# Kernel optimization log

Measured on AMD Instinct MI355X. Metric: run time of the kernel, lower is better.

The kernel has to match this reference:

```python
import jax, jax.numpy as jnp
import numpy as np

THETA_ALPHA = 160.0  # spatial bandwidth of bilateral kernel
THETA_BETA = 3.0     # color bandwidth of bilateral kernel
THETA_GAMMA = 3.0    # spatial bandwidth of spatial kernel
NUM_ITERS = 5        # mean-field iterations


def setup_inputs() -> dict:
    key = jax.random.key(0)
    ks = jax.random.split(key, 5)
    B, H, W, C = 1, 80, 80, 21
    unaries = jax.random.normal(ks[0], (B, H, W, C), dtype=jnp.float32)
    image = jax.random.uniform(ks[1], (B, H, W, 3), dtype=jnp.float32) * 255.0
    spatial_w = jax.random.normal(ks[2], (C, C), dtype=jnp.float32) * 0.1 + jnp.eye(C)
    bilateral_w = jax.random.normal(ks[3], (C, C), dtype=jnp.float32) * 0.1 + jnp.eye(C)
    compat = jax.random.normal(ks[4], (C, C), dtype=jnp.float32) * 0.1 - jnp.eye(C)
    return {"unaries": unaries, "image": image, "spatial_w": spatial_w,
            "bilateral_w": bilateral_w, "compat": compat}


def _gauss_kernel(feat):
    # feat: [N, F] -> dense Gaussian affinity exp(-0.5*||f_i - f_j||^2), [N, N]
    sq = jnp.sum(feat * feat, axis=-1)
    d2 = sq[:, None] + sq[None, :] - 2.0 * (feat @ feat.T)
    return jnp.exp(-0.5 * jnp.maximum(d2, 0.0))


def reference(unaries, image, spatial_w, bilateral_w, compat):
    B, H, W, C = unaries.shape
    N = H * W
    yy, xx = jnp.meshgrid(jnp.arange(H, dtype=jnp.float32),
                          jnp.arange(W, dtype=jnp.float32), indexing="ij")
    pos = jnp.stack([yy, xx], axis=-1).reshape(N, 2)          # [N, 2]
    rgb = image.reshape(N, 3)
    feat_s = pos / THETA_GAMMA                                 # spatial kernel features
    feat_b = jnp.concatenate([pos / THETA_ALPHA, rgb / THETA_BETA], axis=-1)
    Ks = _gauss_kernel(feat_s)                                 # [N, N]
    Kb = _gauss_kernel(feat_b)                                 # [N, N]
    norm_s = jnp.sum(Ks, axis=-1, keepdims=True)               # splat-of-ones normalization
    norm_b = jnp.sum(Kb, axis=-1, keepdims=True)
    u = unaries.reshape(N, C)
    q = u
    for _ in range(NUM_ITERS):
        p = jax.nn.softmax(q, axis=-1)                         # [N, C]
        msg = (Ks @ p) / norm_s @ spatial_w.T + (Kb @ p) / norm_b @ bilateral_w.T
        q = u - msg @ compat.T                                 # compatibility transform
    return q.reshape(B, H, W, C)
```

## Files before the change

kernel.cpp:

```cpp
#include <hip/hip_runtime.h>


#define HH 80
#define WW 80
#define NPIX 6400
#define CC 21
#define PP 24
#define NITER 5
#define NCAP 64
#define SCAP 48
#define SADGATE 23u
#define RAD 14

typedef short short8 __attribute__((ext_vector_type(8)));
union H8 { short8 v; unsigned short u[8]; };

__device__ __forceinline__ float bf2f(unsigned short h) {
    return __uint_as_float(((unsigned)h) << 16);
}
__device__ __forceinline__ unsigned short f2bf(float f) {
    unsigned u = __float_as_uint(f);
    return (unsigned short)((u + 0x7fffu + ((u >> 16) & 1u)) >> 16);
}

__global__ void __launch_bounds__(1024) nbr_kernel(const float* __restrict__ image,
        const float* __restrict__ unaries,
        const float* __restrict__ sw, const float* __restrict__ bw,
        const float* __restrict__ ct,
        int* __restrict__ nbr_j, float* __restrict__ nbr_k, int* __restrict__ nbr_cnt,
        float* __restrict__ norm_b, float* __restrict__ Stab,
        float* __restrict__ csw_g, float* __restrict__ cbw_g,
        unsigned short* __restrict__ p0) {
    __shared__ unsigned int cimg[NPIX];
    int tid = threadIdx.x;
    int bid = blockIdx.x;
    for (int px = tid; px < NPIX; px += 1024) {
        float r = image[px * 3 + 0], g = image[px * 3 + 1], b = image[px * 3 + 2];
        unsigned ur = (unsigned)(r + 0.5f), ug = (unsigned)(g + 0.5f), ub = (unsigned)(b + 0.5f);
        cimg[px] = ur | (ug << 8) | (ub << 16);
    }
    if (bid == 0) {
        if (tid < HH) {
            float s = 0.f;
            float t = (float)tid;
            for (int tp = 0; tp < HH; ++tp) {
                float d = t - (float)tp;
                s += __expf(-d * d * (1.0f / 18.0f));
            }
            Stab[tid] = s;
        }
        for (int idx = tid; idx < 2 * CC * CC; idx += 1024) {
            int m = idx % (CC * CC);
            int c = m / CC, k = m % CC;
            const float* wmat = (idx < CC * CC) ? sw : bw;
            float s = 0.f;
            for (int mm = 0; mm < CC; ++mm) s += ct[c * CC + mm] * wmat[mm * CC + k];
            if (idx < CC * CC) csw_g[m] = s; else cbw_g[m] = s;
        }
    }
    __syncthreads();
    int lane = tid & 63;
    int i = bid * 16 + (tid >> 6);
    unsigned ci = cimg[i];
    float eir = image[i * 3 + 0], eig = image[i * 3 + 1], eib = image[i * 3 + 2];
    float yi = (float)(i / WW), xi = (float)(i % WW);
    int base = 0;
    float ksum = 0.f;
    for (int j0 = 0; j0 < NPIX; j0 += 64) {
        int j = j0 + lane;
        unsigned cj = cimg[j];
#if __has_builtin(__builtin_amdgcn_sad_u8)
        unsigned sad = __builtin_amdgcn_sad_u8(ci, cj, 0u);
#else
        int dr = (int)(ci & 255u) - (int)(cj & 255u);
        int dg = (int)((ci >> 8) & 255u) - (int)((cj >> 8) & 255u);
        int db = (int)((ci >> 16) & 255u) - (int)((cj >> 16) & 255u);
        unsigned sad = (unsigned)(abs(dr) + abs(dg) + abs(db));
#endif
        bool pass = (sad <= SADGATE);
        unsigned long long mask = __ballot(pass);
        if (pass) {
            int slot = base + __popcll(mask & ((1ull << lane) - 1ull));
            if (slot < NCAP) {
                float er = eir - image[j * 3 + 0];
                float eg = eig - image[j * 3 + 1];
                float eb = eib - image[j * 3 + 2];
                float dy = (yi - (float)(j / WW)) * (1.0f / 160.0f);
                float dx = (xi - (float)(j % WW)) * (1.0f / 160.0f);
                float d2 = (er * er + eg * eg + eb * eb) * (1.0f / 9.0f) + dy * dy + dx * dx;
                float kk = __expf(-0.5f * d2);
                nbr_j[i * NCAP + slot] = j;
                nbr_k[i * NCAP + slot] = kk;
                ksum += kk;
            }
        }
        base += (int)__popcll(mask);
    }
    for (int off = 32; off > 0; off >>= 1) ksum += __shfl_down(ksum, off, 64);
    if (lane == 0) {
        nbr_cnt[i] = (base < NCAP) ? base : NCAP;
        norm_b[i] = ksum;
    }
    float v = (lane < CC) ? unaries[i * CC + lane] : -1e30f;
    float m = v;
    for (int off = 16; off > 0; off >>= 1) m = fmaxf(m, __shfl_down(m, off, 32));
    m = __shfl(m, 0, 32);
    float e = (lane < CC) ? __expf(v - m) : 0.f;
    float s = e;
    for (int off = 16; off > 0; off >>= 1) s += __shfl_down(s, off, 32);
    s = __shfl(s, 0, 32);
    if (lane < PP) p0[i * PP + lane] = (lane < CC) ? f2bf(e / s) : (unsigned short)0;
}

__global__ void __launch_bounds__(320) iter_kernel(const float* __restrict__ unaries,
        const unsigned short* __restrict__ pc,
        const int* __restrict__ nbr_j, const float* __restrict__ nbr_k,
        const int* __restrict__ nbr_cnt, const float* __restrict__ norm_b,
        const float* __restrict__ Stab,
        const float* __restrict__ csw_g, const float* __restrict__ cbw_g,
        unsigned short* __restrict__ pn, float* __restrict__ out, int last) {
    __shared__ float lcsw[CC * CC], lcbw[CC * CC];
    __shared__ float gl[16];
    __shared__ float cy[38 * PP];
    __shared__ float asb[10 * 25], abb[10 * 25];
    __shared__ int   njl[10][SCAP];
    __shared__ float nkl[10][SCAP];
    __shared__ int   cnt_l[10];
    __shared__ float inv_ns[10];

    int tid = threadIdx.x;
    int y = blockIdx.x >> 3;
    int x0 = (blockIdx.x & 7) * 10;
    int xs = (x0 - RAD > 0) ? x0 - RAD : 0;
    int xe = (x0 + 10 + RAD < WW) ? x0 + 10 + RAD : WW;
    int extw = xe - xs;
    const short8* pc8 = (const short8*)pc;

    for (int idx = tid; idx < 2 * CC * CC; idx += 320) {
        if (idx < CC * CC) lcsw[idx] = csw_g[idx];
        else lcbw[idx - CC * CC] = cbw_g[idx - CC * CC];
    }
    if (tid < 16) { float d = (float)tid; gl[tid] = __expf(-d * d * (1.0f / 18.0f)); }
    if (tid >= 32 && tid < 42) {
        int px = tid - 32;
        int i = y * WW + x0 + px;
        int cnt = nbr_cnt[i]; if (cnt > SCAP) cnt = SCAP;
        cnt_l[px] = cnt;
        inv_ns[px] = 1.0f / (Stab[y] * Stab[x0 + px]);
    }
    for (int idx = tid; idx < 10 * SCAP; idx += 320) {
        int px = idx / SCAP, sl = idx % SCAP;
        int i = y * WW + x0 + px;
        int cnt = nbr_cnt[i]; if (cnt > SCAP) cnt = SCAP;
        if (sl < cnt) {
            njl[px][sl] = nbr_j[i * NCAP + sl];
            nkl[px][sl] = nbr_k[i * NCAP + sl] / norm_b[i];
        }
    }
    __syncthreads();

    if (tid < extw * 3) {
        int col = tid / 3, grp = tid % 3;
        int x = xs + col;
        int ys_ = (y - RAD > 0) ? y - RAD : 0;
        int ye_ = (y + RAD < HH - 1) ? y + RAD : HH - 1;
        float a[8] = {0, 0, 0, 0, 0, 0, 0, 0};
        for (int yp = ys_; yp <= ye_; ++yp) {
            int d = y - yp; if (d < 0) d = -d;
            float g = gl[d];
            H8 h; h.v = pc8[(yp * WW + x) * 3 + grp];
            #pragma unroll
            for (int e = 0; e < 8; ++e) a[e] += g * bf2f(h.u[e]);
        }
        #pragma unroll
        for (int e = 0; e < 8; ++e) cy[col * PP + grp * 8 + e] = a[e];
    }
    __syncthreads();

    int px = tid >> 5, c = tid & 31;
    int x = x0 + px;
    int i = y * WW + x;
    if (c < CC) {
        int q0 = (x - RAD > 0) ? x - RAD : 0;
        int q1 = (x + RAD < WW - 1) ? x + RAD : WW - 1;
        float s = 0.f;
        for (int xp = q0; xp <= q1; ++xp) {
            int d = x - xp; if (d < 0) d = -d;
            s += gl[d] * cy[(xp - xs) * PP + c];
        }
        asb[px * 25 + c] = s * inv_ns[px];
        int cnt = cnt_l[px];
        float ab = 0.f;
        for (int n = 0; n < cnt; ++n)
            ab += nkl[px][n] * bf2f(pc[njl[px][n] * PP + c]);
        abb[px * 25 + c] = ab;
    }
    __syncthreads();

    if (last) {
        if (c < CC) {
            float m = 0.f;
            #pragma unroll
            for (int k = 0; k < CC; ++k)
                m += lcsw[c * CC + k] * asb[px * 25 + k] + lcbw[c * CC + k] * abb[px * 25 + k];
            out[i * CC + c] = unaries[i * CC + c] - m;
        }
    } else {
        float ev = 0.f;
        if (c < CC) {
            float m = 0.f;
            #pragma unroll
            for (int k = 0; k < CC; ++k)
                m += lcsw[c * CC + k] * asb[px * 25 + k] + lcbw[c * CC + k] * abb[px * 25 + k];
            ev = __expf(unaries[i * CC + c] - m);
        }
        float s = ev;
        #pragma unroll
        for (int off = 16; off > 0; off >>= 1) s += __shfl_xor(s, off, 32);
        if (c < CC) pn[i * PP + c] = f2bf(ev / s);
    }
}

extern "C" void kernel_launch(void* const* d_in, const int* in_sizes, int n_in,
                              void* d_out, int out_size, void* d_ws, size_t ws_size,
                              hipStream_t stream) {
    const float* unaries = (const float*)d_in[0];
    const float* image   = (const float*)d_in[1];
    const float* sw      = (const float*)d_in[2];
    const float* bw      = (const float*)d_in[3];
    const float* ct      = (const float*)d_in[4];
    float* out = (float*)d_out;

    char* ws = (char*)d_ws;
    size_t off = 0;
    auto alloc = [&](size_t bytes) -> char* {
        char* p = ws + off;
        off += (bytes + 255) & ~(size_t)255;
        return p;
    };
    int*   nbr_j   = (int*)alloc((size_t)NPIX * NCAP * 4);
    float* nbr_k   = (float*)alloc((size_t)NPIX * NCAP * 4);
    int*   nbr_cnt = (int*)alloc((size_t)NPIX * 4);
    float* norm_b  = (float*)alloc((size_t)NPIX * 4);
    unsigned short* pA = (unsigned short*)alloc((size_t)NPIX * PP * 2);
    unsigned short* pB = (unsigned short*)alloc((size_t)NPIX * PP * 2);
    float* Stab    = (float*)alloc(HH * 4);
    float* csw_g   = (float*)alloc(CC * CC * 4);
    float* cbw_g   = (float*)alloc(CC * CC * 4);
    (void)ws_size;

    nbr_kernel<<<400, 1024, 0, stream>>>(image, unaries, sw, bw, ct,
                                         nbr_j, nbr_k, nbr_cnt, norm_b, Stab,
                                         csw_g, cbw_g, pA);
    unsigned short* pc = pA;
    unsigned short* pn = pB;
    for (int t = 0; t < NITER; ++t) {
        iter_kernel<<<640, 320, 0, stream>>>(unaries, pc, nbr_j, nbr_k, nbr_cnt,
                                             norm_b, Stab, csw_g, cbw_g, pn, out,
                                             (t == NITER - 1) ? 1 : 0);
        unsigned short* tsw = pc; pc = pn; pn = tsw;
    }
}
```

Baseline: 145.7 us.

## Fuse first mean-field iteration into neighbor kernel and shrink neighbor cap

The neighbor-search kernel now also performs the first mean-field iteration. It computes softmax of the unaries on the fly and writes the second-iteration probabilities, so one iteration launch is dropped. The neighbor cap drops from 64 to 32, and normalization is folded into the stored bilateral weights, which removes the norm_b buffer. The iteration kernel now uses 8-pixel tiles with 256 threads, loads neighbor lists into registers and broadcasts them by shuffle, and computes the Gaussian weights with exp instead of a table. The smaller cap may change accuracy for pixels with many neighbors, and the fused first iteration recomputes softmax per neighbor.

```diff
diff --git a/kernel.cpp b/kernel.cpp
--- a/kernel.cpp
+++ b/kernel.cpp
@@ -7,8 +7,7 @@
 #define CC 21
 #define PP 24
 #define NITER 5
-#define NCAP 64
-#define SCAP 48
+#define NCAP 32
 #define SADGATE 23u
 #define RAD 14
 
@@ -23,152 +22,241 @@
     return (unsigned short)((u + 0x7fffu + ((u >> 16) & 1u)) >> 16);
 }
 
-__global__ void __launch_bounds__(1024) nbr_kernel(const float* __restrict__ image,
+__global__ void __launch_bounds__(1024) nbr0_kernel(const float* __restrict__ image,
         const float* __restrict__ unaries,
         const float* __restrict__ sw, const float* __restrict__ bw,
         const float* __restrict__ ct,
         int* __restrict__ nbr_j, float* __restrict__ nbr_k, int* __restrict__ nbr_cnt,
-        float* __restrict__ norm_b, float* __restrict__ Stab,
-        float* __restrict__ csw_g, float* __restrict__ cbw_g,
-        unsigned short* __restrict__ p0) {
+        float* __restrict__ Stab_g, float* __restrict__ csw_g, float* __restrict__ cbw_g,
+        unsigned short* __restrict__ pn) {
     __shared__ unsigned int cimg[NPIX];
+    __shared__ float Sl[HH];
+    __shared__ float lcsw[CC * CC], lcbw[CC * CC];
+    __shared__ float ms_m[29 * 44], ms_is[29 * 44];
+    __shared__ int   njl[16][NCAP];
+    __shared__ float nkl[16][NCAP];
+    __shared__ int   cnt_l[16];
+    __shared__ float cy[44 * PP];
+    __shared__ float asb[16 * 25], abb[16 * 25];
+
     int tid = threadIdx.x;
     int bid = blockIdx.x;
+    int y = bid / 5;
+    int x0 = (bid % 5) * 16;
+    int xs = (x0 - RAD > 0) ? x0 - RAD : 0;
+    int xe = (x0 + 16 + RAD < WW) ? x0 + 16 + RAD : WW;
+    int extw = xe - xs;
+    int ys_ = (y - RAD > 0) ? y - RAD : 0;
+    int ye_ = (y + RAD < HH - 1) ? y + RAD : HH - 1;
+    int nry = ye_ - ys_ + 1;
+
     for (int px = tid; px < NPIX; px += 1024) {
         float r = image[px * 3 + 0], g = image[px * 3 + 1], b = image[px * 3 + 2];
         unsigned ur = (unsigned)(r + 0.5f), ug = (unsigned)(g + 0.5f), ub = (unsigned)(b + 0.5f);
         cimg[px] = ur | (ug << 8) | (ub << 16);
     }
-    if (bid == 0) {
-        if (tid < HH) {
+    if (tid < HH) {
+        float s = 0.f;
+        float t = (float)tid;
+        for (int tp = 0; tp < HH; ++tp) {
+            float d = t - (float)tp;
+            s += __expf(-d * d * (1.0f / 18.0f));
+        }
+        Sl[tid] = s;
+        if (bid == 0) Stab_g[tid] = s;
+    }
+    for (int idx = tid; idx < 2 * CC * CC; idx += 1024) {
+        int m = idx % (CC * CC);
+        int c = m / CC, k = m % CC;
+        const float* wmat = (idx < CC * CC) ? sw : bw;
+        float s = 0.f;
+        for (int mm = 0; mm < CC; ++mm) s += ct[c * CC + mm] * wmat[mm * CC + k];
+        if (idx < CC * CC) { lcsw[m] = s; if (bid == 0) csw_g[m] = s; }
+        else               { lcbw[m] = s; if (bid == 0) cbw_g[m] = s; }
+    }
+    int npx = nry * extw;
+    for (int idx = tid; idx < npx; idx += 1024) {
+        int j = (ys_ + idx / extw) * WW + xs + idx % extw;
+        float v[CC];
+        float m = -1e30f;
+        #pragma unroll
+        for (int k = 0; k < CC; ++k) { v[k] = unaries[j * CC + k]; m = fmaxf(m, v[k]); }
+        float s = 0.f;
+        #pragma unroll
+        for (int k = 0; k < CC; ++k) s += __expf(v[k] - m);
+        ms_m[idx] = m;
+        ms_is[idx] = 1.0f / s;
+    }
+    __syncthreads();
+
+    int lane = tid & 63;
+    int w = tid >> 6;
+    int i = bid * 16 + w;
+    {
+        unsigned ci = cimg[i];
+        float eir = image[i * 3 + 0], eig = image[i * 3 + 1], eib = image[i * 3 + 2];
+        float yi = (float)(i / WW), xi = (float)(i % WW);
+        int base = 0;
+        float ksum = 0.f;
+        for (int j0 = 0; j0 < NPIX; j0 += 64) {
+            int j = j0 + lane;
+            unsigned cj = cimg[j];
+#if __has_builtin(__builtin_amdgcn_sad_u8)
+            unsigned sad = __builtin_amdgcn_sad_u8(ci, cj, 0u);
+#else
+            int dr = (int)(ci & 255u) - (int)(cj & 255u);
+            int dg = (int)((ci >> 8) & 255u) - (int)((cj >> 8) & 255u);
+            int db = (int)((ci >> 16) & 255u) - (int)((cj >> 16) & 255u);
+            unsigned sad = (unsigned)(abs(dr) + abs(dg) + abs(db));
+#endif
+            bool pass = (sad <= SADGATE);
+            unsigned long long mask = __ballot(pass);
+            if (pass) {
+                int slot = base + __popcll(mask & ((1ull << lane) - 1ull));
+                if (slot < NCAP) {
+                    float er = eir - image[j * 3 + 0];
+                    float eg = eig - image[j * 3 + 1];
+                    float eb = eib - image[j * 3 + 2];
+                    float dy = (yi - (float)(j / WW)) * (1.0f / 160.0f);
+                    float dx = (xi - (float)(j % WW)) * (1.0f / 160.0f);
+                    float d2 = (er * er + eg * eg + eb * eb) * (1.0f / 9.0f) + dy * dy + dx * dx;
+                    float kk = __expf(-0.5f * d2);
+                    njl[w][slot] = j;
+                    nkl[w][slot] = kk;
+                    ksum += kk;
+                }
+            }
+            base += (int)__popcll(mask);
+        }
+        for (int off = 32; off > 0; off >>= 1) ksum += __shfl_down(ksum, off, 64);
+        ksum = __shfl(ksum, 0, 64);
+        int cnt = (base < NCAP) ? base : NCAP;
+        float inv = 1.0f / ksum;
+        if (lane < cnt) {
+            float kv = nkl[w][lane] * inv;
+            nkl[w][lane] = kv;
+            nbr_k[i * NCAP + lane] = kv;
+            nbr_j[i * NCAP + lane] = njl[w][lane];
+        }
+        if (lane == 0) { cnt_l[w] = cnt; nbr_cnt[i] = cnt; }
+    }
+
+    if (tid < extw * 3) {
+        int col = tid / 3, grp = tid % 3;
+        int x = xs + col;
+        int nch = (grp == 2) ? 5 : 8;
+        float a[8] = {0, 0, 0, 0, 0, 0, 0, 0};
+        for (int yp = ys_; yp <= ye_; ++yp) {
+            float d = (float)(y - yp);
+            float g = __expf(-d * d * (1.0f / 18.0f));
+            int hidx = (yp - ys_) * extw + col;
+            float m = ms_m[hidx], is = ms_is[hidx];
+            const float* up = unaries + (yp * WW + x) * CC + grp * 8;
+            #pragma unroll
+            for (int e = 0; e < 8; ++e)
+                if (e < nch) a[e] += g * __expf(up[e] - m) * is;
+        }
+        #pragma unroll
+        for (int e = 0; e < 8; ++e)
+            if (e < nch) cy[col * PP + grp * 8 + e] = a[e];
+    }
+    __syncthreads();
+
+    int px = tid >> 5, c = tid & 31;
+    if (tid < 512) {
+        int x = x0 + px;
+        int ii = y * WW + x;
+        if (c < CC) {
+            int q0 = (x - RAD > 0) ? x - RAD : 0;
+            int q1 = (x + RAD < WW - 1) ? x + RAD : WW - 1;
             float s = 0.f;
-            float t = (float)tid;
-            for (int tp = 0; tp < HH; ++tp) {
-                float d = t - (float)tp;
-                s += __expf(-d * d * (1.0f / 18.0f));
+            for (int xp = q0; xp <= q1; ++xp) {
+                float d = (float)(x - xp);
+                s += __expf(-d * d * (1.0f / 18.0f)) * cy[(xp - xs) * PP + c];
             }
-            Stab[tid] = s;
-        }
-        for (int idx = tid; idx < 2 * CC * CC; idx += 1024) {
-            int m = idx % (CC * CC);
-            int c = m / CC, k = m % CC;
-            const float* wmat = (idx < CC * CC) ? sw : bw;
-            float s = 0.f;
-            for (int mm = 0; mm < CC; ++mm) s += ct[c * CC + mm] * wmat[mm * CC + k];
-            if (idx < CC * CC) csw_g[m] = s; else cbw_g[m] = s;
-        }
-    }
-    __syncthreads();
-    int lane = tid & 63;
-    int i = bid * 16 + (tid >> 6);
-    unsigned ci = cimg[i];
-    float eir = image[i * 3 + 0], eig = image[i * 3 + 1], eib = image[i * 3 + 2];
-    float yi = (float)(i / WW), xi = (float)(i % WW);
-    int base = 0;
-    float ksum = 0.f;
-    for (int j0 = 0; j0 < NPIX; j0 += 64) {
-        int j = j0 + lane;
-        unsigned cj = cimg[j];
-#if __has_builtin(__builtin_amdgcn_sad_u8)
-        unsigned sad = __builtin_amdgcn_sad_u8(ci, cj, 0u);
-#else
-        int dr = (int)(ci & 255u) - (int)(cj & 255u);
-        int dg = (int)((ci >> 8) & 255u) - (int)((cj >> 8) & 255u);
-        int db = (int)((ci >> 16) & 255u) - (int)((cj >> 16) & 255u);
-        unsigned sad = (unsigned)(abs(dr) + abs(dg) + abs(db));
-#endif
-        bool pass = (sad <= SADGATE);
-        unsigned long long mask = __ballot(pass);
-        if (pass) {
-            int slot = base + __popcll(mask & ((1ull << lane) - 1ull));
-            if (slot < NCAP) {
-                float er = eir - image[j * 3 + 0];
-                float eg = eig - image[j * 3 + 1];
-                float eb = eib - image[j * 3 + 2];
-                float dy = (yi - (float)(j / WW)) * (1.0f / 160.0f);
-                float dx = (xi - (float)(j % WW)) * (1.0f / 160.0f);
-                float d2 = (er * er + eg * eg + eb * eb) * (1.0f / 9.0f) + dy * dy + dx * dx;
-                float kk = __expf(-0.5f * d2);
-                nbr_j[i * NCAP + slot] = j;
-                nbr_k[i * NCAP + slot] = kk;
-                ksum += kk;
-            }
-        }
-        base += (int)__popcll(mask);
-    }
-    for (int off = 32; off > 0; off >>= 1) ksum += __shfl_down(ksum, off, 64);
-    if (lane == 0) {
-        nbr_cnt[i] = (base < NCAP) ? base : NCAP;
-        norm_b[i] = ksum;
-    }
-    float v = (lane < CC) ? unaries[i * CC + lane] : -1e30f;
-    float m = v;
-    for (int off = 16; off > 0; off >>= 1) m = fmaxf(m, __shfl_down(m, off, 32));
-    m = __shfl(m, 0, 32);
-    float e = (lane < CC) ? __expf(v - m) : 0.f;
-    float s = e;
-    for (int off = 16; off > 0; off >>= 1) s += __shfl_down(s, off, 32);
-    s = __shfl(s, 0, 32);
-    if (lane < PP) p0[i * PP + lane] = (lane < CC) ? f2bf(e / s) : (unsigned short)0;
-}
-
-__global__ void __launch_bounds__(320) iter_kernel(const float* __restrict__ unaries,
+            asb[px * 25 + c] = s / (Sl[y] * Sl[x]);
+        }
+        int cnt = cnt_l[px];
+        float ab = 0.f;
+        for (int n = 0; n < cnt; ++n) {
+            int j = njl[px][n];
+            float kpre = nkl[px][n];
+            float uv = (c < CC) ? unaries[j * CC + c] : -1e30f;
+            float m = uv;
+            #pragma unroll
+            for (int off = 16; off > 0; off >>= 1) m = fmaxf(m, __shfl_xor(m, off, 32));
+            float e = __expf(uv - m);
+            float s2 = e;
+            #pragma unroll
+            for (int off = 16; off > 0; off >>= 1) s2 += __shfl_xor(s2, off, 32);
+            ab += kpre * e * (1.0f / s2);
+        }
+        if (c < CC) abb[px * 25 + c] = ab;
+        (void)ii;
+    }
+    __syncthreads();
+
+    if (tid < 512) {
+        int x = x0 + px;
+        int ii = y * WW + x;
+        float ev = 0.f;
+        if (c < CC) {
+            float m = 0.f;
+            #pragma unroll
+            for (int k = 0; k < CC; ++k)
+                m += lcsw[c * CC + k] * asb[px * 25 + k] + lcbw[c * CC + k] * abb[px * 25 + k];
+            ev = __expf(unaries[ii * CC + c] - m);
+        }
+        float s = ev;
+        #pragma unroll
+        for (int off = 16; off > 0; off >>= 1) s += __shfl_xor(s, off, 32);
+        if (c < CC) pn[ii * PP + c] = f2bf(ev / s);
+    }
+}
+
+__global__ void __launch_bounds__(256) iter_kernel(const float* __restrict__ unaries,
         const unsigned short* __restrict__ pc,
         const int* __restrict__ nbr_j, const float* __restrict__ nbr_k,
-        const int* __restrict__ nbr_cnt, const float* __restrict__ norm_b,
-        const float* __restrict__ Stab,
+        const int* __restrict__ nbr_cnt,
+        const float* __restrict__ Stab_g,
         const float* __restrict__ csw_g, const float* __restrict__ cbw_g,
         unsigned short* __restrict__ pn, float* __restrict__ out, int last) {
     __shared__ float lcsw[CC * CC], lcbw[CC * CC];
-    __shared__ float gl[16];
-    __shared__ float cy[38 * PP];
-    __shared__ float asb[10 * 25], abb[10 * 25];
-    __shared__ int   njl[10][SCAP];
-    __shared__ float nkl[10][SCAP];
-    __shared__ int   cnt_l[10];
-    __shared__ float inv_ns[10];
+    __shared__ float cy[36 * PP];
+    __shared__ float asb[8 * 25], abb[8 * 25];
 
     int tid = threadIdx.x;
-    int y = blockIdx.x >> 3;
-    int x0 = (blockIdx.x & 7) * 10;
+    int y = blockIdx.x / 10;
+    int x0 = (blockIdx.x % 10) * 8;
     int xs = (x0 - RAD > 0) ? x0 - RAD : 0;
-    int xe = (x0 + 10 + RAD < WW) ? x0 + 10 + RAD : WW;
+    int xe = (x0 + 8 + RAD < WW) ? x0 + 8 + RAD : WW;
     int extw = xe - xs;
     const short8* pc8 = (const short8*)pc;
 
-    for (int idx = tid; idx < 2 * CC * CC; idx += 320) {
+    int px = tid >> 5, c = tid & 31;
+    int x = x0 + px;
+    int i = y * WW + x;
+
+    int   jv = nbr_j[i * NCAP + c];
+    float kv = nbr_k[i * NCAP + c];
+    int   cnt = nbr_cnt[i];
+    float inv_ns = 1.0f / (Stab_g[y] * Stab_g[x]);
+    float u_i = (c < CC) ? unaries[i * CC + c] : 0.f;
+
+    for (int idx = tid; idx < 2 * CC * CC; idx += 256) {
         if (idx < CC * CC) lcsw[idx] = csw_g[idx];
         else lcbw[idx - CC * CC] = cbw_g[idx - CC * CC];
     }
-    if (tid < 16) { float d = (float)tid; gl[tid] = __expf(-d * d * (1.0f / 18.0f)); }
-    if (tid >= 32 && tid < 42) {
-        int px = tid - 32;
-        int i = y * WW + x0 + px;
-        int cnt = nbr_cnt[i]; if (cnt > SCAP) cnt = SCAP;
-        cnt_l[px] = cnt;
-        inv_ns[px] = 1.0f / (Stab[y] * Stab[x0 + px]);
-    }
-    for (int idx = tid; idx < 10 * SCAP; idx += 320) {
-        int px = idx / SCAP, sl = idx % SCAP;
-        int i = y * WW + x0 + px;
-        int cnt = nbr_cnt[i]; if (cnt > SCAP) cnt = SCAP;
-        if (sl < cnt) {
-            njl[px][sl] = nbr_j[i * NCAP + sl];
-            nkl[px][sl] = nbr_k[i * NCAP + sl] / norm_b[i];
-        }
-    }
-    __syncthreads();
-
     if (tid < extw * 3) {
         int col = tid / 3, grp = tid % 3;
-        int x = xs + col;
+        int xa = xs + col;
         int ys_ = (y - RAD > 0) ? y - RAD : 0;
         int ye_ = (y + RAD < HH - 1) ? y + RAD : HH - 1;
         float a[8] = {0, 0, 0, 0, 0, 0, 0, 0};
         for (int yp = ys_; yp <= ye_; ++yp) {
-            int d = y - yp; if (d < 0) d = -d;
-            float g = gl[d];
-            H8 h; h.v = pc8[(yp * WW + x) * 3 + grp];
+            float d = (float)(y - yp);
+            float g = __expf(-d * d * (1.0f / 18.0f));
+            H8 h; h.v = pc8[(yp * WW + xa) * 3 + grp];
             #pragma unroll
             for (int e = 0; e < 8; ++e) a[e] += g * bf2f(h.u[e]);
         }
@@ -177,23 +265,24 @@
     }
     __syncthreads();
 
-    int px = tid >> 5, c = tid & 31;
-    int x = x0 + px;
-    int i = y * WW + x;
     if (c < CC) {
         int q0 = (x - RAD > 0) ? x - RAD : 0;
         int q1 = (x + RAD < WW - 1) ? x + RAD : WW - 1;
         float s = 0.f;
         for (int xp = q0; xp <= q1; ++xp) {
-            int d = x - xp; if (d < 0) d = -d;
-            s += gl[d] * cy[(xp - xs) * PP + c];
-        }
-        asb[px * 25 + c] = s * inv_ns[px];
-        int cnt = cnt_l[px];
+            float d = (float)(x - xp);
+            s += __expf(-d * d * (1.0f / 18.0f)) * cy[(xp - xs) * PP + c];
+        }
+        asb[px * 25 + c] = s * inv_ns;
+    }
+    {
         float ab = 0.f;
-        for (int n = 0; n < cnt; ++n)
-            ab += nkl[px][n] * bf2f(pc[njl[px][n] * PP + c]);
-        abb[px * 25 + c] = ab;
+        for (int n = 0; n < cnt; ++n) {
+            int j = __shfl(jv, n, 32);
+            float kpre = __shfl(kv, n, 32);
+            if (c < CC) ab += kpre * bf2f(pc[j * PP + c]);
+        }
+        if (c < CC) abb[px * 25 + c] = ab;
     }
     __syncthreads();
 
@@ -203,7 +292,7 @@
             #pragma unroll
             for (int k = 0; k < CC; ++k)
                 m += lcsw[c * CC + k] * asb[px * 25 + k] + lcbw[c * CC + k] * abb[px * 25 + k];
-            out[i * CC + c] = unaries[i * CC + c] - m;
+            out[i * CC + c] = u_i - m;
         }
     } else {
         float ev = 0.f;
@@ -212,7 +301,7 @@
             #pragma unroll
             for (int k = 0; k < CC; ++k)
                 m += lcsw[c * CC + k] * asb[px * 25 + k] + lcbw[c * CC + k] * abb[px * 25 + k];
-            ev = __expf(unaries[i * CC + c] - m);
+            ev = __expf(u_i - m);
         }
         float s = ev;
         #pragma unroll
@@ -241,22 +330,21 @@
     int*   nbr_j   = (int*)alloc((size_t)NPIX * NCAP * 4);
     float* nbr_k   = (float*)alloc((size_t)NPIX * NCAP * 4);
     int*   nbr_cnt = (int*)alloc((size_t)NPIX * 4);
-    float* norm_b  = (float*)alloc((size_t)NPIX * 4);
     unsigned short* pA = (unsigned short*)alloc((size_t)NPIX * PP * 2);
     unsigned short* pB = (unsigned short*)alloc((size_t)NPIX * PP * 2);
-    float* Stab    = (float*)alloc(HH * 4);
+    float* Stab_g  = (float*)alloc(HH * 4);
     float* csw_g   = (float*)alloc(CC * CC * 4);
     float* cbw_g   = (float*)alloc(CC * CC * 4);
     (void)ws_size;
 
-    nbr_kernel<<<400, 1024, 0, stream>>>(image, unaries, sw, bw, ct,
-                                         nbr_j, nbr_k, nbr_cnt, norm_b, Stab,
-                                         csw_g, cbw_g, pA);
+    nbr0_kernel<<<400, 1024, 0, stream>>>(image, unaries, sw, bw, ct,
+                                          nbr_j, nbr_k, nbr_cnt,
+                                          Stab_g, csw_g, cbw_g, pA);
     unsigned short* pc = pA;
     unsigned short* pn = pB;
-    for (int t = 0; t < NITER; ++t) {
-        iter_kernel<<<640, 320, 0, stream>>>(unaries, pc, nbr_j, nbr_k, nbr_cnt,
-                                             norm_b, Stab, csw_g, cbw_g, pn, out,
+    for (int t = 1; t < NITER; ++t) {
+        iter_kernel<<<800, 256, 0, stream>>>(unaries, pc, nbr_j, nbr_k, nbr_cnt,
+                                             Stab_g, csw_g, cbw_g, pn, out,
                                              (t == NITER - 1) ? 1 : 0);
         unsigned short* tsw = pc; pc = pn; pn = tsw;
     }
```

After: 161.6 us. 1.11x slower.
